# Optimization experiments

Hardware: AMD Instinct MI355X
Metric: run time of the kernel (lower is better)

The kernel has to match this reference:

```python
import jax, jax.numpy as jnp
import numpy as np

GROUPS = 32
HEADS = 8
EPS = 1e-5


def group_norm(x, w, b):
    B, C, H, W = x.shape
    xg = x.reshape(B, GROUPS, C // GROUPS, H, W)
    mu = xg.mean(axis=(2, 3, 4), keepdims=True)
    var = xg.var(axis=(2, 3, 4), keepdims=True)
    xn = ((xg - mu) * jax.lax.rsqrt(var + EPS)).reshape(B, C, H, W)
    return xn * w[None, :, None, None] + b[None, :, None, None]


def conv1x1(x, w, b):
    # w: [out_c, in_c], x: [B, C, H, W]
    return jnp.einsum('oc,bchw->bohw', w, x) + b[None, :, None, None]


def setup_inputs() -> dict:
    key = jax.random.key(0)
    ks = jax.random.split(key, 10)
    B, C, H, W = 8, 512, 32, 32
    s = 1.0 / np.sqrt(C)
    inp = {
        'x': jax.random.normal(ks[0], (B, C, H, W), dtype=jnp.float32),
        'gn_w': jnp.ones((C,), jnp.float32),
        'gn_b': jnp.zeros((C,), jnp.float32),
        'qw': jax.random.uniform(ks[1], (C, C), jnp.float32, -s, s),
        'qb': jax.random.uniform(ks[2], (C,), jnp.float32, -s, s),
        'kw': jax.random.uniform(ks[3], (C, C), jnp.float32, -s, s),
        'kb': jax.random.uniform(ks[4], (C,), jnp.float32, -s, s),
        'vw': jax.random.uniform(ks[5], (C, C), jnp.float32, -s, s),
        'vb': jax.random.uniform(ks[6], (C,), jnp.float32, -s, s),
        'ow': jax.random.uniform(ks[7], (C, C), jnp.float32, -s, s),
        'ob': jax.random.uniform(ks[8], (C,), jnp.float32, -s, s),
    }
    return inp


def reference(x, gn_w, gn_b, qw, qb, kw, kb, vw, vb, ow, ob):
    B, C, H, W = x.shape
    hd = C // HEADS          # head_dim
    N = H * W                # spatial tokens
    scale = float(hd) ** -0.5

    xn = group_norm(x, gn_w, gn_b)
    q = conv1x1(xn, qw, qb).reshape(B, HEADS, hd, N)
    k = conv1x1(xn, kw, kb).reshape(B, HEADS, hd, N)
    v = conv1x1(xn, vw, vb).reshape(B, HEADS, hd, N)

    # scores[b,h,n,m] = scale * <q[:, :, :, n], k[:, :, :, m]>
    scores = jnp.einsum('bhdn,bhdm->bhnm', q * scale, k)
    attn = jax.nn.softmax(scores, axis=-1)
    # out[b,h,d,n] = sum_m attn[b,h,n,m] * v[b,h,d,m]
    out = jnp.einsum('bhnm,bhdm->bhdn', attn, v).reshape(B, C, H, W)
    out = conv1x1(out, ow, ob)
    return out + x
```

## Files before the change

kernel.cpp:

```cpp
#include <hip/hip_runtime.h>
#include <cstdint>


typedef unsigned short u16;
typedef __attribute__((ext_vector_type(8))) __bf16 bf16x8;
typedef __attribute__((ext_vector_type(4))) __bf16 bf16x4;
typedef __attribute__((ext_vector_type(4))) float  f32x4;

typedef __attribute__((address_space(1))) const unsigned int guint;
typedef __attribute__((address_space(3))) unsigned int       luint;

__device__ __forceinline__ u16 f2bf(float f) {
  union { float f; unsigned u; } a; a.f = f;
  unsigned r = a.u + 0x7fffu + ((a.u >> 16) & 1u);
  return (u16)(r >> 16);
}

__device__ __forceinline__ void gload16(u16* lds_dst, const u16* g_src) {
  __builtin_amdgcn_global_load_lds((guint*)g_src, (luint*)lds_dst, 16, 0, 0);
}

__global__ __launch_bounds__(256) void gn_kernel(const float* __restrict__ x,
                                                 const float* __restrict__ gw,
                                                 const float* __restrict__ gb,
                                                 u16* __restrict__ xnT) {
  int b = blockIdx.x >> 5, g = blockIdx.x & 31;
  int tid = threadIdx.x;
  const float* xg = x + ((size_t)b * 512 + g * 16) * 1024;
  float s1 = 0.f, s2 = 0.f;
  for (int i = tid; i < 16384; i += 256) {
    int c = i >> 10, n = i & 1023;
    float v = xg[c * 1024 + n];
    s1 += v; s2 += v * v;
  }
#pragma unroll
  for (int d = 32; d; d >>= 1) { s1 += __shfl_down(s1, d, 64); s2 += __shfl_down(s2, d, 64); }
  __shared__ float redw[4][2];
  if ((tid & 63) == 0) { redw[tid >> 6][0] = s1; redw[tid >> 6][1] = s2; }
  __syncthreads();
  float t1 = redw[0][0] + redw[1][0] + redw[2][0] + redw[3][0];
  float t2 = redw[0][1] + redw[1][1] + redw[2][1] + redw[3][1];
  float mean = t1 * (1.f / 16384.f);
  float var  = t2 * (1.f / 16384.f) - mean * mean;
  float rinv = rsqrtf(var + 1e-5f);
  int c = tid & 15;
  int cg = g * 16 + c;
  float wgt = gw[cg] * rinv;
  float bia = gb[cg] - mean * wgt;
  u16* dst = xnT + (size_t)b * 524288 + cg;
  const float* xc = xg + c * 1024;
  for (int i = tid; i < 16384; i += 256) {
    int n = i >> 4;
    dst[(size_t)n * 512] = f2bf(xc[n] * wgt + bia);
  }
}

__global__ __launch_bounds__(256) void cvtw_kernel(const float* __restrict__ q,
                                                   const float* __restrict__ k,
                                                   const float* __restrict__ v,
                                                   const float* __restrict__ o,
                                                   u16* __restrict__ dst) {
  int i = blockIdx.x * 256 + threadIdx.x;
  int wsel = i >> 16;
  const float* src = wsel == 0 ? q : wsel == 1 ? k : wsel == 2 ? v : o;
  f32x4 val = *(const f32x4*)(src + (size_t)(i & 65535) * 4);
  u16 r0 = f2bf(val[0]), r1 = f2bf(val[1]), r2 = f2bf(val[2]), r3 = f2bf(val[3]);
  unsigned lo = (unsigned)r0 | ((unsigned)r1 << 16);
  unsigned hi = (unsigned)r2 | ((unsigned)r3 << 16);
  unsigned long long pk = (unsigned long long)lo | ((unsigned long long)hi << 32);
  *(unsigned long long*)(dst + (size_t)i * 4) = pk;
}

__global__ __launch_bounds__(256) void gemm_qkv(
    const u16* __restrict__ xnT, const u16* __restrict__ Wc,
    const float* __restrict__ qb, const float* __restrict__ kb,
    const float* __restrict__ vb,
    u16* __restrict__ Qs, u16* __restrict__ Ks, u16* __restrict__ Vs) {
  __shared__ u16 smem[32768];
  int id = blockIdx.x;
  int xcd = id & 7, slot = id >> 3;
  int g12 = slot / 12, q12 = slot % 12;
  int p = xcd * 8 + g12;
  int b = p & 7, yt = p >> 3;
  int xt = q12 & 3, which = q12 >> 2;

  const u16* Ab = xnT + (size_t)b * 524288 + (size_t)yt * 128 * 512;
  const u16* Bb = Wc + which * 262144 + (size_t)xt * 128 * 512;
  const float* bias = which == 0 ? qb : (which == 1 ? kb : vb);
  float scale = which == 0 ? 0.18033688011112043f : 1.0f;

  int tid = threadIdx.x, w = tid >> 6, lane = tid & 63;
  int wr = w >> 1, wcn = w & 1;
  int srow = lane >> 3, sk8 = (lane & 7) ^ srow;
  f32x4 acc[4][4] = {};

#define QKV_STAGE(buf, k0)                                                     \
  {                                                                            \
    u16* lA_ = smem + (buf) * 8192;                                            \
    u16* lB_ = smem + 16384 + (buf) * 8192;                                    \
    _Pragma("unroll")                                                          \
    for (int c2 = 0; c2 < 4; ++c2) {                                           \
      int ck = w * 4 + c2;                                                     \
      gload16(&lA_[ck * 512], Ab + (size_t)(ck * 8 + srow) * 512 + (k0) + sk8 * 8); \
      gload16(&lB_[ck * 512], Bb + (size_t)(ck * 8 + srow) * 512 + (k0) + sk8 * 8); \
    }                                                                          \
  }

  QKV_STAGE(0, 0);
  __syncthreads();
  for (int t = 0; t < 8; ++t) {
    if (t < 7) QKV_STAGE((t + 1) & 1, (t + 1) * 64);
    const u16* lA = smem + (t & 1) * 8192;
    const u16* lB = smem + 16384 + (t & 1) * 8192;
#pragma unroll
    for (int ks = 0; ks < 2; ++ks) {
      int k8 = ks * 4 + (lane >> 4);
      bf16x8 af[4], bfr[4];
#pragma unroll
      for (int mf = 0; mf < 4; ++mf) {
        int row = wr * 64 + mf * 16 + (lane & 15);
        af[mf] = *(const bf16x8*)&lA[row * 64 + ((k8 ^ (row & 7)) * 8)];
      }
#pragma unroll
      for (int nf = 0; nf < 4; ++nf) {
        int row = wcn * 64 + nf * 16 + (lane & 15);
        bfr[nf] = *(const bf16x8*)&lB[row * 64 + ((k8 ^ (row & 7)) * 8)];
      }
#pragma unroll
      for (int mf = 0; mf < 4; ++mf)
#pragma unroll
        for (int nf = 0; nf < 4; ++nf)
          acc[mf][nf] = __builtin_amdgcn_mfma_f32_16x16x32_bf16(af[mf], bfr[nf], acc[mf][nf], 0, 0, 0);
    }
    __syncthreads();
  }
#undef QKV_STAGE

  if (which < 2) {
    u16* dst = (which == 0 ? Qs : Ks) + (size_t)b * 524288;
#pragma unroll
    for (int mf = 0; mf < 4; ++mf)
#pragma unroll
      for (int nf = 0; nf < 4; ++nf) {
        int cc = xt * 128 + wcn * 64 + nf * 16 + (lane & 15);
        float bv = bias[cc];
#pragma unroll
        for (int j = 0; j < 4; ++j) {
          int rr = yt * 128 + wr * 64 + mf * 16 + (lane >> 4) * 4 + j;
          dst[(size_t)rr * 512 + cc] = f2bf((acc[mf][nf][j] + bv) * scale);
        }
      }
  } else {
    u16* tr = smem;
#pragma unroll
    for (int mf = 0; mf < 4; ++mf)
#pragma unroll
      for (int nf = 0; nf < 4; ++nf) {
        int cc_t = wcn * 64 + nf * 16 + (lane & 15);
        float bv = bias[xt * 128 + cc_t];
#pragma unroll
        for (int j = 0; j < 4; ++j) {
          int rr_t = wr * 64 + mf * 16 + (lane >> 4) * 4 + j;
          tr[cc_t * 136 + rr_t] = f2bf(acc[mf][nf][j] + bv);
        }
      }
    __syncthreads();
    int r = tid >> 1, half = tid & 1;
    size_t base = (size_t)b * 524288 + (size_t)(xt * 128 + r) * 1024 + yt * 128 + half * 64;
#pragma unroll
    for (int i = 0; i < 8; ++i) {
      bf16x8 v = *(const bf16x8*)&tr[r * 136 + half * 64 + i * 8];
      *(bf16x8*)&Vs[base + i * 8] = v;
    }
  }
}

__global__ __launch_bounds__(256) void attn_kernel(const u16* __restrict__ Q,
                                                   const u16* __restrict__ Kt,
                                                   const u16* __restrict__ V,
                                                   u16* __restrict__ AO) {
  __shared__ u16 lK[2][4096];
  __shared__ u16 lV[2][4096];
  __shared__ u16 plds[4][1024];
  int id = blockIdx.x;
  int xcd = id & 7, slot = id >> 3;
  int bh = xcd * 8 + (slot >> 4);
  int ntile = slot & 15;
  int b = bh >> 3, h = bh & 7;
  int tid = threadIdx.x, w = tid >> 6, lane = tid & 63;
  int ln = lane & 15, hi = lane >> 4;
  int nb = ntile * 64 + w * 16;
  const u16* Qb = Q  + (size_t)b * 524288;
  const u16* Kb = Kt + (size_t)b * 524288 + h * 64;
  const u16* Vb = V  + (size_t)b * 524288 + (size_t)(h * 64) * 1024;
  char* pw = (char*)&plds[w][0];
  int srow = lane >> 3, sk8 = (lane & 7) ^ srow;

  int kidx[2][4];
#pragma unroll
  for (int ks = 0; ks < 2; ++ks)
#pragma unroll
    for (int xf = 0; xf < 4; ++xf) {
      int row = xf * 16 + ln;
      kidx[ks][xf] = row * 64 + (((ks * 4 + hi) ^ (row & 7)) * 8);
    }
  int woff[4], roff[2];
#pragma unroll
  for (int nf = 0; nf < 4; ++nf)
    woff[nf] = ln * 128 + ((nf * 32 + hi * 8) ^ ((ln & 7) << 4));
#pragma unroll
  for (int ks = 0; ks < 2; ++ks)
    roff[ks] = ln * 128 + ((ks * 64 + hi * 16) ^ ((ln & 7) << 4));

  bf16x8 bq[2];
#pragma unroll
  for (int ks = 0; ks < 2; ++ks)
    bq[ks] = *(const bf16x8*)&Qb[(size_t)(nb + ln) * 512 + h * 64 + ks * 32 + hi * 8];

  f32x4 o[4] = {};
  float lpart = 0.f;

#define ATTN_STAGE(buf, m0)                                                    \
  {                                                                            \
    _Pragma("unroll")                                                          \
    for (int c2 = 0; c2 < 2; ++c2) {                                           \
      int ck = w * 2 + c2;                                                     \
      gload16(&lK[buf][ck * 512], Kb + (size_t)((m0) + ck * 8 + srow) * 512 + sk8 * 8); \
      gload16(&lV[buf][ck * 512], Vb + (size_t)(ck * 8 + srow) * 1024 + (m0) + sk8 * 8); \
    }                                                                          \
  }

  ATTN_STAGE(0, 0);
  __syncthreads();
  for (int mt = 0; mt < 16; ++mt) {
    int cur = mt & 1;
    if (mt < 15) ATTN_STAGE(cur ^ 1, (mt + 1) * 64);
    f32x4 s[4] = {};
#pragma unroll
    for (int ks = 0; ks < 2; ++ks) {
#pragma unroll
      for (int nf = 0; nf < 4; ++nf) {
        bf16x8 ak = *(const bf16x8*)&lK[cur][kidx[ks][nf]];
        s[nf] = __builtin_amdgcn_mfma_f32_16x16x32_bf16(ak, bq[ks], s[nf], 0, 0, 0);
      }
    }
#pragma unroll
    for (int nf = 0; nf < 4; ++nf) {
      float p0 = exp2f(s[nf][0]), p1 = exp2f(s[nf][1]);
      float p2 = exp2f(s[nf][2]), p3 = exp2f(s[nf][3]);
      lpart += (p0 + p1) + (p2 + p3);
      bf16x4 pb;
      pb[0] = (__bf16)p0; pb[1] = (__bf16)p1; pb[2] = (__bf16)p2; pb[3] = (__bf16)p3;
      *(bf16x4*)(pw + woff[nf]) = pb;
    }
#pragma unroll
    for (int ks = 0; ks < 2; ++ks) {
      bf16x8 ap = *(const bf16x8*)(pw + roff[ks]);
#pragma unroll
      for (int df = 0; df < 4; ++df) {
        bf16x8 bv = *(const bf16x8*)&lV[cur][kidx[ks][df]];
        o[df] = __builtin_amdgcn_mfma_f32_16x16x32_bf16(ap, bv, o[df], 0, 0, 0);
      }
    }
    __syncthreads();
  }
#undef ATTN_STAGE

  lpart += __shfl_xor(lpart, 16, 64);
  lpart += __shfl_xor(lpart, 32, 64);
  float* lf = (float*)pw;
  if (hi == 0) lf[ln] = lpart;
  f32x4 lv = *(const f32x4*)&lf[hi * 4];
  float rl[4];
#pragma unroll
  for (int j = 0; j < 4; ++j) rl[j] = 1.0f / lv[j];

#pragma unroll
  for (int df = 0; df < 4; ++df)
#pragma unroll
    for (int j = 0; j < 4; ++j) {
      int n = nb + hi * 4 + j;
      int c = h * 64 + df * 16 + ln;
      AO[(size_t)b * 524288 + (size_t)n * 512 + c] = f2bf(o[df][j] * rl[j]);
    }
}

__global__ __launch_bounds__(256) void gemm_proj(
    const u16* __restrict__ Wo, const u16* __restrict__ AO,
    const float* __restrict__ ob, const float* __restrict__ x,
    float* __restrict__ out) {
  __shared__ u16 smem[24576];
  int id = blockIdx.x;
  int xcd = id & 7, slot = id >> 3;
  int g8 = slot >> 3, y = slot & 7;
  int p = xcd * 8 + g8;
  int b = p & 7, xt = p >> 3;

  const u16* Ab = Wo + (size_t)y * 64 * 512;
  const u16* Bb = AO + (size_t)b * 524288 + (size_t)xt * 128 * 512;

  int tid = threadIdx.x, w = tid >> 6, lane = tid & 63;
  int wr = w >> 1, wcn = w & 1;
  int srow = lane >> 3, sk8 = (lane & 7) ^ srow;
  f32x4 acc[2][4] = {};

#define PROJ_STAGE(buf, k0)                                                    \
  {                                                                            \
    u16* lA_ = smem + (buf) * 4096;                                            \
    u16* lB_ = smem + 8192 + (buf) * 8192;                                     \
    _Pragma("unroll")                                                          \
    for (int c2 = 0; c2 < 6; ++c2) {                                           \
      int ck = w * 6 + c2;                                                     \
      if (ck < 8)                                                              \
        gload16(&lA_[ck * 512], Ab + (size_t)(ck * 8 + srow) * 512 + (k0) + sk8 * 8); \
      else                                                                     \
        gload16(&lB_[(ck - 8) * 512], Bb + (size_t)((ck - 8) * 8 + srow) * 512 + (k0) + sk8 * 8); \
    }                                                                          \
  }

  PROJ_STAGE(0, 0);
  __syncthreads();
  for (int t = 0; t < 8; ++t) {
    if (t < 7) PROJ_STAGE((t + 1) & 1, (t + 1) * 64);
    const u16* lA = smem + (t & 1) * 4096;
    const u16* lB = smem + 8192 + (t & 1) * 8192;
#pragma unroll
    for (int ks = 0; ks < 2; ++ks) {
      int k8 = ks * 4 + (lane >> 4);
      bf16x8 af[2], bfr[4];
#pragma unroll
      for (int mf = 0; mf < 2; ++mf) {
        int row = wr * 32 + mf * 16 + (lane & 15);
        af[mf] = *(const bf16x8*)&lA[row * 64 + ((k8 ^ (row & 7)) * 8)];
      }
#pragma unroll
      for (int nf = 0; nf < 4; ++nf) {
        int row = wcn * 64 + nf * 16 + (lane & 15);
        bfr[nf] = *(const bf16x8*)&lB[row * 64 + ((k8 ^ (row & 7)) * 8)];
      }
#pragma unroll
      for (int mf = 0; mf < 2; ++mf)
#pragma unroll
        for (int nf = 0; nf < 4; ++nf)
          acc[mf][nf] = __builtin_amdgcn_mfma_f32_16x16x32_bf16(af[mf], bfr[nf], acc[mf][nf], 0, 0, 0);
    }
    __syncthreads();
  }
#undef PROJ_STAGE

#pragma unroll
  for (int mf = 0; mf < 2; ++mf)
#pragma unroll
    for (int nf = 0; nf < 4; ++nf) {
      int cc = xt * 128 + wcn * 64 + nf * 16 + (lane & 15);
#pragma unroll
      for (int j = 0; j < 4; ++j) {
        int rr = y * 64 + wr * 32 + mf * 16 + (lane >> 4) * 4 + j;
        size_t idx = (size_t)b * 524288 + (size_t)rr * 1024 + cc;
        out[idx] = acc[mf][nf][j] + ob[rr] + x[idx];
      }
    }
}

extern "C" void kernel_launch(void* const* d_in, const int* in_sizes, int n_in,
                              void* d_out, int out_size, void* d_ws, size_t ws_size,
                              hipStream_t stream) {
  const float* x   = (const float*)d_in[0];
  const float* gnw = (const float*)d_in[1];
  const float* gnb = (const float*)d_in[2];
  const float* qw  = (const float*)d_in[3];
  const float* qb  = (const float*)d_in[4];
  const float* kw  = (const float*)d_in[5];
  const float* kb  = (const float*)d_in[6];
  const float* vw  = (const float*)d_in[7];
  const float* vb  = (const float*)d_in[8];
  const float* ow  = (const float*)d_in[9];
  const float* ob  = (const float*)d_in[10];
  float* out = (float*)d_out;

  u16* ws  = (u16*)d_ws;
  u16* xnT = ws;
  u16* Qs  = ws + 4194304;
  u16* Ks  = ws + 8388608;
  u16* Vs  = ws + 12582912;
  u16* Wc  = ws + 16777216;
  u16* AO  = xnT;

  gn_kernel<<<256, 256, 0, stream>>>(x, gnw, gnb, xnT);
  cvtw_kernel<<<1024, 256, 0, stream>>>(qw, kw, vw, ow, Wc);
  gemm_qkv<<<768, 256, 0, stream>>>(xnT, Wc, qb, kb, vb, Qs, Ks, Vs);
  attn_kernel<<<1024, 256, 0, stream>>>(Qs, Ks, Vs, AO);
  gemm_proj<<<512, 256, 0, stream>>>(Wc + 786432, AO, ob, x, out);
}
```

Before: 185.3 us.

## Split group norm into stats/apply kernels and double attention query tile per wave

```diff
diff --git a/kernel.cpp b/kernel.cpp
--- a/kernel.cpp
+++ b/kernel.cpp
@@ -20,39 +20,66 @@
   __builtin_amdgcn_global_load_lds((guint*)g_src, (luint*)lds_dst, 16, 0, 0);
 }
 
-__global__ __launch_bounds__(256) void gn_kernel(const float* __restrict__ x,
-                                                 const float* __restrict__ gw,
-                                                 const float* __restrict__ gb,
-                                                 u16* __restrict__ xnT) {
-  int b = blockIdx.x >> 5, g = blockIdx.x & 31;
+__global__ __launch_bounds__(256) void gn_stats(const float* __restrict__ x,
+                                                float* __restrict__ pstat) {
+  int id = blockIdx.x;
+  int bg = id >> 1, chunk = id & 1;
+  int b = bg >> 5, g = bg & 31;
   int tid = threadIdx.x;
-  const float* xg = x + ((size_t)b * 512 + g * 16) * 1024;
+  const float* xg = x + ((size_t)(b * 512 + g * 16 + chunk * 8)) * 1024;
   float s1 = 0.f, s2 = 0.f;
-  for (int i = tid; i < 16384; i += 256) {
-    int c = i >> 10, n = i & 1023;
-    float v = xg[c * 1024 + n];
-    s1 += v; s2 += v * v;
+#pragma unroll
+  for (int it = 0; it < 8; ++it) {
+    f32x4 v = *(const f32x4*)(xg + it * 1024 + tid * 4);
+    s1 += (v[0] + v[1]) + (v[2] + v[3]);
+    s2 += (v[0] * v[0] + v[1] * v[1]) + (v[2] * v[2] + v[3] * v[3]);
   }
 #pragma unroll
   for (int d = 32; d; d >>= 1) { s1 += __shfl_down(s1, d, 64); s2 += __shfl_down(s2, d, 64); }
   __shared__ float redw[4][2];
   if ((tid & 63) == 0) { redw[tid >> 6][0] = s1; redw[tid >> 6][1] = s2; }
   __syncthreads();
-  float t1 = redw[0][0] + redw[1][0] + redw[2][0] + redw[3][0];
-  float t2 = redw[0][1] + redw[1][1] + redw[2][1] + redw[3][1];
-  float mean = t1 * (1.f / 16384.f);
-  float var  = t2 * (1.f / 16384.f) - mean * mean;
+  if (tid == 0) {
+    float t1 = redw[0][0] + redw[1][0] + redw[2][0] + redw[3][0];
+    float t2 = redw[0][1] + redw[1][1] + redw[2][1] + redw[3][1];
+    pstat[(bg * 2 + chunk) * 2 + 0] = t1;
+    pstat[(bg * 2 + chunk) * 2 + 1] = t2;
+  }
+}
+
+__global__ __launch_bounds__(256) void gn_apply(const float* __restrict__ x,
+                                                const float* __restrict__ pstat,
+                                                const float* __restrict__ gw,
+                                                const float* __restrict__ gb,
+                                                u16* __restrict__ xnT) {
+  __shared__ u16 tr[64 * 130];
+  int id = blockIdx.x;
+  int cs = id & 3, ntl = (id >> 2) & 15, b = id >> 6;
+  int tid = threadIdx.x;
+  int tc = tid >> 1, th = tid & 1;
+  int c = cs * 128 + tc, g = c >> 4;
+  float a1 = pstat[(b * 32 + g) * 4 + 0], a2 = pstat[(b * 32 + g) * 4 + 1];
+  float b1 = pstat[(b * 32 + g) * 4 + 2], b2 = pstat[(b * 32 + g) * 4 + 3];
+  float s1 = a1 + b1, s2 = a2 + b2;
+  float mean = s1 * (1.f / 16384.f);
+  float var  = s2 * (1.f / 16384.f) - mean * mean;
   float rinv = rsqrtf(var + 1e-5f);
-  int c = tid & 15;
-  int cg = g * 16 + c;
-  float wgt = gw[cg] * rinv;
-  float bia = gb[cg] - mean * wgt;
-  u16* dst = xnT + (size_t)b * 524288 + cg;
-  const float* xc = xg + c * 1024;
-  for (int i = tid; i < 16384; i += 256) {
-    int n = i >> 4;
-    dst[(size_t)n * 512] = f2bf(xc[n] * wgt + bia);
-  }
+  float wgt = gw[c] * rinv;
+  float bia = gb[c] - mean * wgt;
+  const float* src = x + ((size_t)(b * 512 + c)) * 1024 + ntl * 64 + th * 32;
+#pragma unroll
+  for (int i = 0; i < 8; ++i) {
+    f32x4 v = *(const f32x4*)(src + i * 4);
+#pragma unroll
+    for (int j = 0; j < 4; ++j)
+      tr[(th * 32 + i * 4 + j) * 130 + tc] = f2bf(v[j] * wgt + bia);
+  }
+  __syncthreads();
+  int n = tid >> 2, q = tid & 3;
+  u16* dst = xnT + (size_t)b * 524288 + (size_t)(ntl * 64 + n) * 512 + cs * 128 + q * 32;
+#pragma unroll
+  for (int wd = 0; wd < 16; ++wd)
+    *(unsigned*)&dst[wd * 2] = *(const unsigned*)&tr[n * 130 + q * 32 + wd * 2];
 }
 
 __global__ __launch_bounds__(256) void cvtw_kernel(const float* __restrict__ q,
@@ -179,17 +206,17 @@
                                                    const u16* __restrict__ Kt,
                                                    const u16* __restrict__ V,
                                                    u16* __restrict__ AO) {
-  __shared__ u16 lK[2][4096];
-  __shared__ u16 lV[2][4096];
-  __shared__ u16 plds[4][1024];
+  __shared__ __align__(16) u16 lK[2][4096];
+  __shared__ __align__(16) u16 lV[2][4096];
+  __shared__ __align__(16) u16 plds[4][2048];
   int id = blockIdx.x;
   int xcd = id & 7, slot = id >> 3;
-  int bh = xcd * 8 + (slot >> 4);
-  int ntile = slot & 15;
+  int bh = xcd * 8 + (slot >> 3);
+  int nt = slot & 7;
   int b = bh >> 3, h = bh & 7;
   int tid = threadIdx.x, w = tid >> 6, lane = tid & 63;
   int ln = lane & 15, hi = lane >> 4;
-  int nb = ntile * 64 + w * 16;
+  int nb = nt * 128 + w * 32;
   const u16* Qb = Q  + (size_t)b * 524288;
   const u16* Kb = Kt + (size_t)b * 524288 + h * 64;
   const u16* Vb = V  + (size_t)b * 524288 + (size_t)(h * 64) * 1024;
@@ -212,13 +239,16 @@
   for (int ks = 0; ks < 2; ++ks)
     roff[ks] = ln * 128 + ((ks * 64 + hi * 16) ^ ((ln & 7) << 4));
 
-  bf16x8 bq[2];
-#pragma unroll
-  for (int ks = 0; ks < 2; ++ks)
-    bq[ks] = *(const bf16x8*)&Qb[(size_t)(nb + ln) * 512 + h * 64 + ks * 32 + hi * 8];
-
-  f32x4 o[4] = {};
-  float lpart = 0.f;
+  bf16x8 bq[2][2];
+#pragma unroll
+  for (int nq = 0; nq < 2; ++nq)
+#pragma unroll
+    for (int ks = 0; ks < 2; ++ks)
+      bq[nq][ks] = *(const bf16x8*)&Qb[(size_t)(nb + nq * 16 + ln) * 512 +
+                                       h * 64 + ks * 32 + hi * 8];
+
+  f32x4 o[2][4] = {};
+  float lp[2] = {0.f, 0.f};
 
 #define ATTN_STAGE(buf, m0)                                                    \
   {                                                                            \
@@ -235,54 +265,65 @@
   for (int mt = 0; mt < 16; ++mt) {
     int cur = mt & 1;
     if (mt < 15) ATTN_STAGE(cur ^ 1, (mt + 1) * 64);
-    f32x4 s[4] = {};
+    f32x4 s[2][4] = {};
 #pragma unroll
     for (int ks = 0; ks < 2; ++ks) {
 #pragma unroll
       for (int nf = 0; nf < 4; ++nf) {
         bf16x8 ak = *(const bf16x8*)&lK[cur][kidx[ks][nf]];
-        s[nf] = __builtin_amdgcn_mfma_f32_16x16x32_bf16(ak, bq[ks], s[nf], 0, 0, 0);
-      }
-    }
-#pragma unroll
-    for (int nf = 0; nf < 4; ++nf) {
-      float p0 = exp2f(s[nf][0]), p1 = exp2f(s[nf][1]);
-      float p2 = exp2f(s[nf][2]), p3 = exp2f(s[nf][3]);
-      lpart += (p0 + p1) + (p2 + p3);
-      bf16x4 pb;
-      pb[0] = (__bf16)p0; pb[1] = (__bf16)p1; pb[2] = (__bf16)p2; pb[3] = (__bf16)p3;
-      *(bf16x4*)(pw + woff[nf]) = pb;
-    }
+        s[0][nf] = __builtin_amdgcn_mfma_f32_16x16x32_bf16(ak, bq[0][ks], s[0][nf], 0, 0, 0);
+        s[1][nf] = __builtin_amdgcn_mfma_f32_16x16x32_bf16(ak, bq[1][ks], s[1][nf], 0, 0, 0);
+      }
+    }
+#pragma unroll
+    for (int nq = 0; nq < 2; ++nq)
+#pragma unroll
+      for (int nf = 0; nf < 4; ++nf) {
+        float p0 = exp2f(s[nq][nf][0]), p1 = exp2f(s[nq][nf][1]);
+        float p2 = exp2f(s[nq][nf][2]), p3 = exp2f(s[nq][nf][3]);
+        lp[nq] += (p0 + p1) + (p2 + p3);
+        bf16x4 pb;
+        pb[0] = (__bf16)p0; pb[1] = (__bf16)p1; pb[2] = (__bf16)p2; pb[3] = (__bf16)p3;
+        *(bf16x4*)(pw + nq * 2048 + woff[nf]) = pb;
+      }
 #pragma unroll
     for (int ks = 0; ks < 2; ++ks) {
-      bf16x8 ap = *(const bf16x8*)(pw + roff[ks]);
+      bf16x8 ap0 = *(const bf16x8*)(pw + roff[ks]);
+      bf16x8 ap1 = *(const bf16x8*)(pw + 2048 + roff[ks]);
 #pragma unroll
       for (int df = 0; df < 4; ++df) {
         bf16x8 bv = *(const bf16x8*)&lV[cur][kidx[ks][df]];
-        o[df] = __builtin_amdgcn_mfma_f32_16x16x32_bf16(ap, bv, o[df], 0, 0, 0);
+        o[0][df] = __builtin_amdgcn_mfma_f32_16x16x32_bf16(ap0, bv, o[0][df], 0, 0, 0);
+        o[1][df] = __builtin_amdgcn_mfma_f32_16x16x32_bf16(ap1, bv, o[1][df], 0, 0, 0);
       }
     }
     __syncthreads();
   }
 #undef ATTN_STAGE
 
-  lpart += __shfl_xor(lpart, 16, 64);
-  lpart += __shfl_xor(lpart, 32, 64);
+#pragma unroll
+  for (int nq = 0; nq < 2; ++nq) {
+    lp[nq] += __shfl_xor(lp[nq], 16, 64);
+    lp[nq] += __shfl_xor(lp[nq], 32, 64);
+  }
   float* lf = (float*)pw;
-  if (hi == 0) lf[ln] = lpart;
-  f32x4 lv = *(const f32x4*)&lf[hi * 4];
-  float rl[4];
-#pragma unroll
-  for (int j = 0; j < 4; ++j) rl[j] = 1.0f / lv[j];
-
-#pragma unroll
-  for (int df = 0; df < 4; ++df)
-#pragma unroll
-    for (int j = 0; j < 4; ++j) {
-      int n = nb + hi * 4 + j;
-      int c = h * 64 + df * 16 + ln;
-      AO[(size_t)b * 524288 + (size_t)n * 512 + c] = f2bf(o[df][j] * rl[j]);
-    }
+  if (hi == 0) { lf[ln] = lp[0]; lf[16 + ln] = lp[1]; }
+  f32x4 lv0 = *(const f32x4*)&lf[hi * 4];
+  f32x4 lv1 = *(const f32x4*)&lf[16 + hi * 4];
+  float rl[2][4];
+#pragma unroll
+  for (int j = 0; j < 4; ++j) { rl[0][j] = 1.0f / lv0[j]; rl[1][j] = 1.0f / lv1[j]; }
+
+#pragma unroll
+  for (int nq = 0; nq < 2; ++nq)
+#pragma unroll
+    for (int df = 0; df < 4; ++df)
+#pragma unroll
+      for (int j = 0; j < 4; ++j) {
+        int n = nb + nq * 16 + hi * 4 + j;
+        int c = h * 64 + df * 16 + ln;
+        AO[(size_t)b * 524288 + (size_t)n * 512 + c] = f2bf(o[nq][df][j] * rl[nq][j]);
+      }
 }
 
 __global__ __launch_bounds__(256) void gemm_proj(
@@ -384,11 +425,13 @@
   u16* Ks  = ws + 8388608;
   u16* Vs  = ws + 12582912;
   u16* Wc  = ws + 16777216;
+  float* pstat = (float*)(ws + 17825792);
   u16* AO  = xnT;
 
-  gn_kernel<<<256, 256, 0, stream>>>(x, gnw, gnb, xnT);
+  gn_stats<<<512, 256, 0, stream>>>(x, pstat);
+  gn_apply<<<512, 256, 0, stream>>>(x, pstat, gnw, gnb, xnT);
   cvtw_kernel<<<1024, 256, 0, stream>>>(qw, kw, vw, ow, Wc);
   gemm_qkv<<<768, 256, 0, stream>>>(xnT, Wc, qb, kb, vb, Qs, Ks, Vs);
-  attn_kernel<<<1024, 256, 0, stream>>>(Qs, Ks, Vs, AO);
+  attn_kernel<<<512, 256, 0, stream>>>(Qs, Ks, Vs, AO);
   gemm_proj<<<512, 256, 0, stream>>>(Wc + 786432, AO, ob, x, out);
 }
```

New measurement: 165.8 us. -10.6%, faster.
